# Optimization experiments

Measured on AMD Instinct MI355X. Metric: run time of the kernel, lower is better.

The kernel has to match this reference:

```python
import jax, jax.numpy as jnp
import numpy as np

N = 50000          # nodes
E = 800000         # edges
D_IN = 768         # LM embedding dim (hardcoded in SimpleHGN first conv)
H = 128            # hidden_dim
REL_DIM = 32       # hardcoded rel_dim
N_REL = 3          # n_relations
BETA = 0.05        # SimpleHGN_att_res
NEG_SLOPE = 0.2    # LeakyReLU in attention


def setup_inputs() -> dict:
    key = jax.random.key(0)
    ks = jax.random.split(key, 16)
    s = 0.05  # param init scale
    return {
        'x': jax.random.normal(ks[0], (N, D_IN), jnp.float32),
        'edge_index': jax.random.randint(ks[1], (2, E), 0, N, dtype=jnp.int64),
        'edge_type': jax.random.randint(ks[2], (E,), 0, N_REL, dtype=jnp.int64),
        'W0': jax.random.normal(ks[3], (D_IN, H), jnp.float32) * s,
        'Wr0': jax.random.normal(ks[4], (REL_DIM, H), jnp.float32) * s,
        'a0': jax.random.normal(ks[5], (3 * H, 1), jnp.float32) * s,
        'rel0': jax.random.normal(ks[6], (N_REL, REL_DIM), jnp.float32) * s,
        'W1': jax.random.normal(ks[7], (H, H), jnp.float32) * s,
        'Wr1': jax.random.normal(ks[8], (REL_DIM, H), jnp.float32) * s,
        'a1': jax.random.normal(ks[9], (3 * H, 1), jnp.float32) * s,
        'rel1': jax.random.normal(ks[10], (N_REL, REL_DIM), jnp.float32) * s,
        'pool_w': jax.random.normal(ks[11], (H, H), jnp.float32) * s,
        'pool_b': jnp.zeros((H,), jnp.float32),
        'out_w': jax.random.normal(ks[12], (H, 2), jnp.float32) * s,
        'out_b': jnp.zeros((2,), jnp.float32),
    }


def _hgn_conv(x, src, dst, et, W, Wr, a, rel, pre_alpha):
    """One SimpleHGNConv layer. Returns (ELU(aggregated), alpha detached)."""
    h = x @ W                                   # [N, H]
    r = rel[et] @ Wr                            # [E, H] edge-type embedding
    aw = a[:, 0]
    a_i, a_j, a_r = aw[:h.shape[1]], aw[h.shape[1]:2 * h.shape[1]], aw[2 * h.shape[1]:]
    # logits = leaky_relu(cat(h_i, h_j, r) @ a) computed without [E,3H] concat
    node_i = h @ a_i                            # [N]
    node_j = h @ a_j                            # [N]
    logit = jax.nn.leaky_relu(node_i[dst] + node_j[src] + r @ a_r, NEG_SLOPE)  # [E]
    # segment softmax over destination node neighborhoods (PyG softmax, +1e-16)
    m = jax.ops.segment_max(logit, dst, num_segments=N)
    e = jnp.exp(logit - m[dst])
    ssum = jax.ops.segment_sum(e, dst, num_segments=N)
    alpha = e / (ssum[dst] + 1e-16)             # [E]
    if pre_alpha is not None:
        alpha = alpha * (1.0 - BETA) + pre_alpha * BETA
    msg = h[src] * alpha[:, None]               # [E, H]
    out = jax.ops.segment_sum(msg, dst, num_segments=N)  # [N, H]
    return jax.nn.elu(out), jax.lax.stop_gradient(alpha)


def reference(x, edge_index, edge_type, W0, Wr0, a0, rel0, W1, Wr1, a1, rel1,
              pool_w, pool_b, out_w, out_b):
    src, dst = edge_index[0], edge_index[1]     # x_j = source, x_i = target
    h, alpha = _hgn_conv(x, src, dst, edge_type, W0, Wr0, a0, rel0, None)
    h, alpha = _hgn_conv(h, src, dst, edge_type, W1, Wr1, a1, rel1, alpha)
    # dropout is identity in eval; activation = relu per config
    h = jax.nn.relu(h @ pool_w + pool_b)
    return h @ out_w + out_b                    # [N, 2]
```

## Files before the change

kernel.cpp:

```cpp
#include <hip/hip_runtime.h>
#include <hip/hip_fp16.h>
#include <cstdint>
#include <cstddef>

#define N_NODES 50000
#define N_EDGES 800000
#define DIN_    768
#define H_DIM   128
#define N_REL   3
#define BETA_F  0.05f
#define SLOPE_F 0.2f

static inline int cdiv(int a, int b) { return (a + b - 1) / b; }

typedef __attribute__((ext_vector_type(8))) short bf16x8;
typedef __attribute__((ext_vector_type(8))) unsigned short u16x8;
typedef __attribute__((ext_vector_type(4))) float f32x4;

__device__ __forceinline__ unsigned short f2bf(float f) {
  unsigned u = __builtin_bit_cast(unsigned, f);
  unsigned r = (u + 0x7fffu + ((u >> 16) & 1u)) >> 16;
  return (unsigned short)r;
}
__device__ __forceinline__ float bf2f(unsigned short h) {
  unsigned u = ((unsigned)h) << 16;
  return __builtin_bit_cast(float, u);
}

#define GLOAD_LDS16(g, s) __builtin_amdgcn_global_load_lds( \
    (const __attribute__((address_space(1))) void*)(g),      \
    (__attribute__((address_space(3))) void*)(s), 16, 0, 0)

__global__ void k_count(const int* __restrict__ dst, int* __restrict__ deg, int E) {
  int e = blockIdx.x * blockDim.x + threadIdx.x;
  if (e < E) atomicAdd(&deg[dst[e]], 1);
}

__global__ __launch_bounds__(256) void k_scan1(const int* __restrict__ deg,
                                               int* __restrict__ part, int n) {
  __shared__ int wsum[4];
  int i = blockIdx.x * 256 + threadIdx.x;
  int lane = threadIdx.x & 63, w = threadIdx.x >> 6;
  int v = (i < n) ? deg[i] : 0;
  #pragma unroll
  for (int d = 32; d > 0; d >>= 1) v += __shfl_xor(v, d);
  if (lane == 0) wsum[w] = v;
  __syncthreads();
  if (threadIdx.x == 0) part[blockIdx.x] = wsum[0] + wsum[1] + wsum[2] + wsum[3];
}

__global__ __launch_bounds__(256) void k_scan2(int* __restrict__ part,
                                               int* __restrict__ off, int nb, int n) {
  __shared__ int sh[256];
  int t = threadIdx.x;
  int v = (t < nb) ? part[t] : 0;
  int incl = v;
  sh[t] = incl;
  __syncthreads();
  #pragma unroll
  for (int d = 1; d < 256; d <<= 1) {
    int u = (t >= d) ? sh[t - d] : 0;
    __syncthreads();
    sh[t] += u;
    __syncthreads();
  }
  incl = sh[t];
  if (t < nb) part[t] = incl - v;
  if (t == nb - 1) off[n] = incl;
}

__global__ __launch_bounds__(256) void k_scan3(const int* __restrict__ deg,
                                               const int* __restrict__ part,
                                               int* __restrict__ off,
                                               int* __restrict__ cur, int n) {
  __shared__ int wsum[4];
  int i = blockIdx.x * 256 + threadIdx.x;
  int lane = threadIdx.x & 63, w = threadIdx.x >> 6;
  int v = (i < n) ? deg[i] : 0;
  int incl = v;
  #pragma unroll
  for (int d = 1; d < 64; d <<= 1) {
    int u = __shfl_up(incl, d);
    if (lane >= d) incl += u;
  }
  if (lane == 63) wsum[w] = incl;
  __syncthreads();
  int woff = 0;
  #pragma unroll
  for (int k = 0; k < 4; ++k) woff += (k < w) ? wsum[k] : 0;
  int ex = incl - v + woff + part[blockIdx.x];
  if (i < n) { off[i] = ex; cur[i] = ex; }
}

__global__ void k_fill(const int* __restrict__ dst, int* __restrict__ cur,
                       int* __restrict__ csr, int E) {
  int e = blockIdx.x * blockDim.x + threadIdx.x;
  if (e < E) {
    int p = atomicAdd(&cur[dst[e]], 1);
    csr[p] = e;
  }
}

__global__ __launch_bounds__(128) void k_relscore(const float* __restrict__ rel,
                                                  const float* __restrict__ Wr,
                                                  const float* __restrict__ a,
                                                  float* __restrict__ rs) {
  __shared__ float red[128];
  int k = threadIdx.x;
  for (int t = 0; t < N_REL; ++t) {
    float p = 0.f;
    #pragma unroll
    for (int j = 0; j < 32; ++j) p += rel[t * 32 + j] * Wr[j * H_DIM + k];
    red[k] = p * a[2 * H_DIM + k];
    __syncthreads();
    for (int s = 64; s > 0; s >>= 1) {
      if (k < s) red[k] += red[k + s];
      __syncthreads();
    }
    if (k == 0) rs[t] = red[0];
    __syncthreads();
  }
}

__global__ void k_prep(const float* __restrict__ W, int K,
                       short* __restrict__ th, short* __restrict__ tl) {
  int id = blockIdx.x * 256 + threadIdx.x;
  if (id >= K * 128) return;
  int k = id >> 7, c = id & 127;
  float w = W[id];
  unsigned short h = f2bf(w);
  unsigned short l = f2bf(w - bf2f(h));
  int kt = k >> 5;
  int kk = k & 31;
  int g = kk >> 3, j = kk & 7;
  int p = g ^ (c & 3) ^ ((c >> 2) & 3);
  size_t pos = (size_t)kt * 4096 + c * 32 + p * 8 + j;
  th[pos] = (short)h;
  tl[pos] = (short)l;
}

template <bool BIASRELU, bool W16>
__global__ __launch_bounds__(256, 5) void k_gemm_mfma(const float* __restrict__ A,
                                                      const short* __restrict__ Bth,
                                                      const short* __restrict__ Btl,
                                                      const float* __restrict__ bias,
                                                      float* __restrict__ C,
                                                      __half* __restrict__ C16,
                                                      int n, int K) {
  __shared__ __align__(16) char sm[2][16384];
  int t = threadIdx.x;
  int l = t & 63, wid = t >> 6;
  int wr = wid >> 1, wc = wid & 1;
  int lr = l & 15, lk = l >> 4;
  int row0 = blockIdx.x * 64;

  f32x4 acc[2][4];
  #pragma unroll
  for (int m = 0; m < 2; ++m)
    #pragma unroll
    for (int nn = 0; nn < 4; ++nn) acc[m][nn] = (f32x4)(0.f);

  const int nt = K >> 5;

  const float* a_src0;
  const float* a_src1;
  {
    int s = wid;
    int r = s * 8 + (l >> 3);
    int gr = row0 + r; if (gr >= n) gr = n - 1;
    a_src0 = A + (size_t)gr * K + (((l & 7) ^ (r & 7)) << 2);
    s = 4 + wid;
    r = s * 8 + (l >> 3);
    gr = row0 + r; if (gr >= n) gr = n - 1;
    a_src1 = A + (size_t)gr * K + (((l & 7) ^ (r & 7)) << 2);
  }

  auto stage = [&](int it, char* buf) {
    int k0 = it << 5;
    const short* bh_t = Bth + (size_t)it * 4096;
    GLOAD_LDS16(a_src0 + k0,                    buf + wid * 1024);
    GLOAD_LDS16(a_src1 + k0,                    buf + (4 + wid) * 1024);
    GLOAD_LDS16(bh_t + wid * 512 + l * 8,       buf + 8192 + wid * 1024);
    GLOAD_LDS16(bh_t + (4 + wid) * 512 + l * 8, buf + 8192 + (4 + wid) * 1024);
  };

  auto compute = [&](int it, const char* buf) {
    const char* Ab = buf;
    const char* Bhb = buf + 8192;
    const short* bl_t = Btl + (size_t)it * 4096;
    bf16x8 ah[2], al[2], bh[4], bl[4];
    #pragma unroll
    for (int m = 0; m < 2; ++m) {
      int r = wr * 32 + m * 16 + lr;
      int g0 = (2 * lk) ^ (r & 7);
      int g1 = (2 * lk + 1) ^ (r & 7);
      float4 f0 = *(const float4*)(Ab + r * 128 + g0 * 16);
      float4 f1 = *(const float4*)(Ab + r * 128 + g1 * 16);
      float ff[8] = {f0.x, f0.y, f0.z, f0.w, f1.x, f1.y, f1.z, f1.w};
      u16x8 hv, lv;
      #pragma unroll
      for (int j = 0; j < 8; ++j) {
        unsigned u = __builtin_bit_cast(unsigned, ff[j]);
        unsigned short h = (unsigned short)(u >> 16);
        hv[j] = h;
        lv[j] = f2bf(ff[j] - bf2f(h));
      }
      ah[m] = __builtin_bit_cast(bf16x8, hv);
      al[m] = __builtin_bit_cast(bf16x8, lv);
    }
    #pragma unroll
    for (int nn = 0; nn < 4; ++nn) {
      int c = wc * 64 + nn * 16 + lr;
      int p = lk ^ (c & 3) ^ ((c >> 2) & 3);
      bh[nn] = *(const bf16x8*)(Bhb + c * 64 + p * 16);
      bl[nn] = *(const bf16x8*)(bl_t + c * 32 + p * 8);
    }
    #pragma unroll
    for (int m = 0; m < 2; ++m)
      #pragma unroll
      for (int nn = 0; nn < 4; ++nn) {
        acc[m][nn] = __builtin_amdgcn_mfma_f32_16x16x32_bf16(ah[m], bh[nn], acc[m][nn], 0, 0, 0);
        acc[m][nn] = __builtin_amdgcn_mfma_f32_16x16x32_bf16(ah[m], bl[nn], acc[m][nn], 0, 0, 0);
        acc[m][nn] = __builtin_amdgcn_mfma_f32_16x16x32_bf16(al[m], bh[nn], acc[m][nn], 0, 0, 0);
      }
  };

  stage(0, sm[0]);
  if (nt > 1) stage(1, sm[1]);

  for (int it = 0; it < nt; ++it) {
    if (it + 1 < nt) { asm volatile("s_waitcnt vmcnt(4)" ::: "memory"); }
    else             { asm volatile("s_waitcnt vmcnt(0)" ::: "memory"); }
    asm volatile("s_barrier" ::: "memory");
    compute(it, sm[it & 1]);
    asm volatile("s_barrier" ::: "memory");
    if (it + 2 < nt) stage(it + 2, sm[it & 1]);
  }

  #pragma unroll
  for (int m = 0; m < 2; ++m) {
    int rbase = row0 + wr * 32 + m * 16 + lk * 4;
    #pragma unroll
    for (int nn = 0; nn < 4; ++nn) {
      int c = wc * 64 + nn * 16 + lr;
      #pragma unroll
      for (int q = 0; q < 4; ++q) {
        int r = rbase + q;
        if (r < n) {
          float v = acc[m][nn][q];
          if (BIASRELU) {
            v += bias[c];
            v = v > 0.f ? v : 0.f;
          }
          C[(size_t)r * 128 + c] = v;
          if (W16) C16[(size_t)r * 128 + c] = __float2half(v);
        }
      }
    }
  }
}

__global__ __launch_bounds__(256) void k_scores(const float* __restrict__ h,
                                                const float* __restrict__ a,
                                                float* __restrict__ ni,
                                                float* __restrict__ nj, int n) {
  int lane = threadIdx.x & 63;
  int w = threadIdx.x >> 6;
  int row = blockIdx.x * 4 + w;
  if (row >= n) return;
  float2 v = ((const float2*)(h + (size_t)row * H_DIM))[lane];
  float2 ai = ((const float2*)a)[lane];
  float2 aj = ((const float2*)(a + H_DIM))[lane];
  float si = v.x * ai.x + v.y * ai.y;
  float sj = v.x * aj.x + v.y * aj.y;
  #pragma unroll
  for (int d = 32; d > 0; d >>= 1) {
    si += __shfl_xor(si, d);
    sj += __shfl_xor(sj, d);
  }
  if (lane == 0) { ni[row] = si; nj[row] = sj; }
}

__global__ void k_logit(const int* __restrict__ src, const int* __restrict__ dst,
                        const int* __restrict__ et,
                        const float* __restrict__ ni, const float* __restrict__ nj,
                        const float* __restrict__ rs,
                        float* __restrict__ logit, int E) {
  int e = blockIdx.x * blockDim.x + threadIdx.x;
  if (e >= E) return;
  float v = ni[dst[e]] + nj[src[e]] + rs[et[e]];
  logit[e] = v > 0.f ? v : SLOPE_F * v;
}

template <int LAYER>
__global__ __launch_bounds__(128) void k_aggregate(const int* __restrict__ off,
                                                   const int* __restrict__ csr,
                                                   const int* __restrict__ src,
                                                   const float* __restrict__ logit,
                                                   const __half* __restrict__ h16,
                                                   float* __restrict__ alpha_io,
                                                   float* __restrict__ hout, int n) {
  __shared__ float l_red[2];
  __shared__ float l_alpha[128];
  __shared__ int   l_src[128];
  int nid = blockIdx.x;
  int t = threadIdx.x;
  int lane = t & 63;
  int w = t >> 6;
  int start = off[nid];
  int deg = off[nid + 1] - start;
  float hv = 0.f;
  if (deg > 0) {
    float m = -INFINITY;
    for (int k = t; k < deg; k += 128) m = fmaxf(m, logit[csr[start + k]]);
    #pragma unroll
    for (int d = 32; d > 0; d >>= 1) m = fmaxf(m, __shfl_xor(m, d));
    if (lane == 0) l_red[w] = m;
    __syncthreads();
    m = fmaxf(l_red[0], l_red[1]);
    __syncthreads();
    float s = 0.f;
    for (int k = t; k < deg; k += 128) s += expf(logit[csr[start + k]] - m);
    #pragma unroll
    for (int d = 32; d > 0; d >>= 1) s += __shfl_xor(s, d);
    if (lane == 0) l_red[w] = s;
    __syncthreads();
    float denom = l_red[0] + l_red[1] + 1e-16f;
    for (int base = 0; base < deg; base += 128) {
      int kk = base + t;
      if (kk < deg) {
        int e = csr[start + kk];
        float al = expf(logit[e] - m) / denom;
        if (LAYER == 1) {
          al = al * (1.f - BETA_F) + BETA_F * alpha_io[e];
        } else {
          alpha_io[e] = al;
        }
        l_alpha[t] = al;
        l_src[t] = src[e];
      }
      __syncthreads();
      int cnt = deg - base; if (cnt > 128) cnt = 128;
      #pragma unroll 4
      for (int k = 0; k < cnt; ++k)
        hv += l_alpha[k] * __half2float(h16[(size_t)l_src[k] * H_DIM + t]);
      __syncthreads();
    }
  }
  hout[(size_t)nid * H_DIM + t] = hv > 0.f ? hv : expm1f(hv);
}

__global__ __launch_bounds__(256) void k_out(const float* __restrict__ P,
                                             const float* __restrict__ ow,
                                             const float* __restrict__ ob,
                                             float* __restrict__ out, int n) {
  int lane = threadIdx.x & 63;
  int w = threadIdx.x >> 6;
  int row = blockIdx.x * 4 + w;
  if (row >= n) return;
  float2 v  = ((const float2*)(P + (size_t)row * H_DIM))[lane];
  float2 w0 = ((const float2*)ow)[2 * lane];
  float2 w1 = ((const float2*)ow)[2 * lane + 1];
  float s0 = v.x * w0.x + v.y * w1.x;
  float s1 = v.x * w0.y + v.y * w1.y;
  #pragma unroll
  for (int d = 32; d > 0; d >>= 1) {
    s0 += __shfl_xor(s0, d);
    s1 += __shfl_xor(s1, d);
  }
  if (lane == 0) {
    out[row * 2]     = s0 + ob[0];
    out[row * 2 + 1] = s1 + ob[1];
  }
}

extern "C" void kernel_launch(void* const* d_in, const int* in_sizes, int n_in,
                              void* d_out, int out_size, void* d_ws, size_t ws_size,
                              hipStream_t stream) {
  const float* x      = (const float*)d_in[0];
  const int*   ei     = (const int*)d_in[1];
  const int*   et     = (const int*)d_in[2];
  const float* W0     = (const float*)d_in[3];
  const float* Wr0    = (const float*)d_in[4];
  const float* a0     = (const float*)d_in[5];
  const float* rel0   = (const float*)d_in[6];
  const float* W1     = (const float*)d_in[7];
  const float* Wr1    = (const float*)d_in[8];
  const float* a1     = (const float*)d_in[9];
  const float* rel1   = (const float*)d_in[10];
  const float* pool_w = (const float*)d_in[11];
  const float* pool_b = (const float*)d_in[12];
  const float* out_w  = (const float*)d_in[13];
  const float* out_b  = (const float*)d_in[14];

  const int* src = ei;
  const int* dst = ei + N_EDGES;

  char* p = (char*)d_ws;
  auto take = [&](size_t bytes) {
    char* r = p;
    p += (bytes + 511) & ~(size_t)511;
    return r;
  };
  int*   deg    = (int*)take((size_t)N_NODES * 4);
  int*   off    = (int*)take((size_t)(N_NODES + 1) * 4);
  int*   cur    = (int*)take((size_t)N_NODES * 4);
  int*   part   = (int*)take((size_t)256 * 4);
  int*   csr    = (int*)take((size_t)N_EDGES * 4);
  float* logit  = (float*)take((size_t)N_EDGES * 4);
  float* alpha0 = (float*)take((size_t)N_EDGES * 4);
  float* ni     = (float*)take((size_t)N_NODES * 4);
  float* nj     = (float*)take((size_t)N_NODES * 4);
  float* rs     = (float*)take(256);
  short* wt0h   = (short*)take((size_t)DIN_ * 128 * 2);
  short* wt0l   = (short*)take((size_t)DIN_ * 128 * 2);
  short* wt1h   = (short*)take((size_t)128 * 128 * 2);
  short* wt1l   = (short*)take((size_t)128 * 128 * 2);
  short* wph    = (short*)take((size_t)128 * 128 * 2);
  short* wpl    = (short*)take((size_t)128 * 128 * 2);
  float* big1   = (float*)take((size_t)N_NODES * H_DIM * 4);
  float* big2   = (float*)take((size_t)N_NODES * H_DIM * 4);
  __half* h16   = (__half*)take((size_t)N_NODES * H_DIM * 2);

  const int EB = cdiv(N_EDGES, 256);
  const int GB = cdiv(N_NODES, 64);
  const int SB = cdiv(N_NODES, 256);

  hipMemsetAsync(deg, 0, (size_t)N_NODES * 4, stream);
  k_count<<<EB, 256, 0, stream>>>(dst, deg, N_EDGES);
  k_scan1<<<SB, 256, 0, stream>>>(deg, part, N_NODES);
  k_scan2<<<1, 256, 0, stream>>>(part, off, SB, N_NODES);
  k_scan3<<<SB, 256, 0, stream>>>(deg, part, off, cur, N_NODES);
  k_fill<<<EB, 256, 0, stream>>>(dst, cur, csr, N_EDGES);

  k_prep<<<cdiv(DIN_ * 128, 256), 256, 0, stream>>>(W0, DIN_, wt0h, wt0l);
  k_prep<<<cdiv(128 * 128, 256), 256, 0, stream>>>(W1, 128, wt1h, wt1l);
  k_prep<<<cdiv(128 * 128, 256), 256, 0, stream>>>(pool_w, 128, wph, wpl);

  k_relscore<<<1, 128, 0, stream>>>(rel0, Wr0, a0, rs);
  k_gemm_mfma<false, true><<<GB, 256, 0, stream>>>(x, wt0h, wt0l, nullptr, big1, h16, N_NODES, DIN_);
  k_scores<<<cdiv(N_NODES, 4), 256, 0, stream>>>(big1, a0, ni, nj, N_NODES);
  k_logit<<<EB, 256, 0, stream>>>(src, dst, et, ni, nj, rs, logit, N_EDGES);
  k_aggregate<0><<<N_NODES, 128, 0, stream>>>(off, csr, src, logit, h16, alpha0, big2, N_NODES);

  k_relscore<<<1, 128, 0, stream>>>(rel1, Wr1, a1, rs);
  k_gemm_mfma<false, true><<<GB, 256, 0, stream>>>(big2, wt1h, wt1l, nullptr, big1, h16, N_NODES, 128);
  k_scores<<<cdiv(N_NODES, 4), 256, 0, stream>>>(big1, a1, ni, nj, N_NODES);
  k_logit<<<EB, 256, 0, stream>>>(src, dst, et, ni, nj, rs, logit, N_EDGES);
  k_aggregate<1><<<N_NODES, 128, 0, stream>>>(off, csr, src, logit, h16, alpha0, big2, N_NODES);

  k_gemm_mfma<true, false><<<GB, 256, 0, stream>>>(big2, wph, wpl, pool_b, big1, nullptr, N_NODES, 128);
  k_out<<<cdiv(N_NODES, 4), 256, 0, stream>>>(big1, out_w, out_b, (float*)d_out, N_NODES);
}
```

Before: 433.9 us.

## Store edge data in CSR order and stage low-part weights through LDS

k_fill now records each edge's CSR position and writes a CSR-sorted source array. k_logit scatters logits directly into CSR order, so k_aggregate reads logits, sources and alpha contiguously instead of through a csr indirection. Separately, the GEMM also stages the low bf16 weight tile into LDS, which enlarges shared memory and lowers launch bounds from 5 to 3 blocks per CU. This trades random gathers in the aggregation for a scattered write in k_logit and an extra position array. The GEMM change risks lower occupancy.

Result: faster. 381.6 us (-12.0%).

```diff
diff --git a/kernel.cpp b/kernel.cpp
--- a/kernel.cpp
+++ b/kernel.cpp
@@ -92,12 +92,14 @@
   if (i < n) { off[i] = ex; cur[i] = ex; }
 }
 
-__global__ void k_fill(const int* __restrict__ dst, int* __restrict__ cur,
-                       int* __restrict__ csr, int E) {
+__global__ void k_fill(const int* __restrict__ dst, const int* __restrict__ src,
+                       int* __restrict__ cur, int* __restrict__ pos,
+                       int* __restrict__ src_s, int E) {
   int e = blockIdx.x * blockDim.x + threadIdx.x;
   if (e < E) {
     int p = atomicAdd(&cur[dst[e]], 1);
-    csr[p] = e;
+    pos[e] = p;
+    src_s[p] = src[e];
   }
 }
 
@@ -140,14 +142,14 @@
 }
 
 template <bool BIASRELU, bool W16>
-__global__ __launch_bounds__(256, 5) void k_gemm_mfma(const float* __restrict__ A,
+__global__ __launch_bounds__(256, 3) void k_gemm_mfma(const float* __restrict__ A,
                                                       const short* __restrict__ Bth,
                                                       const short* __restrict__ Btl,
                                                       const float* __restrict__ bias,
                                                       float* __restrict__ C,
                                                       __half* __restrict__ C16,
                                                       int n, int K) {
-  __shared__ __align__(16) char sm[2][16384];
+  __shared__ __align__(16) char sm[2][24576];
   int t = threadIdx.x;
   int l = t & 63, wid = t >> 6;
   int wr = wid >> 1, wc = wid & 1;
@@ -178,16 +180,19 @@
   auto stage = [&](int it, char* buf) {
     int k0 = it << 5;
     const short* bh_t = Bth + (size_t)it * 4096;
+    const short* bl_t = Btl + (size_t)it * 4096;
     GLOAD_LDS16(a_src0 + k0,                    buf + wid * 1024);
     GLOAD_LDS16(a_src1 + k0,                    buf + (4 + wid) * 1024);
     GLOAD_LDS16(bh_t + wid * 512 + l * 8,       buf + 8192 + wid * 1024);
     GLOAD_LDS16(bh_t + (4 + wid) * 512 + l * 8, buf + 8192 + (4 + wid) * 1024);
+    GLOAD_LDS16(bl_t + wid * 512 + l * 8,       buf + 16384 + wid * 1024);
+    GLOAD_LDS16(bl_t + (4 + wid) * 512 + l * 8, buf + 16384 + (4 + wid) * 1024);
   };
 
-  auto compute = [&](int it, const char* buf) {
+  auto compute = [&](const char* buf) {
     const char* Ab = buf;
     const char* Bhb = buf + 8192;
-    const short* bl_t = Btl + (size_t)it * 4096;
+    const char* Blb = buf + 16384;
     bf16x8 ah[2], al[2], bh[4], bl[4];
     #pragma unroll
     for (int m = 0; m < 2; ++m) {
@@ -213,7 +218,7 @@
       int c = wc * 64 + nn * 16 + lr;
       int p = lk ^ (c & 3) ^ ((c >> 2) & 3);
       bh[nn] = *(const bf16x8*)(Bhb + c * 64 + p * 16);
-      bl[nn] = *(const bf16x8*)(bl_t + c * 32 + p * 8);
+      bl[nn] = *(const bf16x8*)(Blb + c * 64 + p * 16);
     }
     #pragma unroll
     for (int m = 0; m < 2; ++m)
@@ -229,10 +234,10 @@
   if (nt > 1) stage(1, sm[1]);
 
   for (int it = 0; it < nt; ++it) {
-    if (it + 1 < nt) { asm volatile("s_waitcnt vmcnt(4)" ::: "memory"); }
+    if (it + 1 < nt) { asm volatile("s_waitcnt vmcnt(6)" ::: "memory"); }
     else             { asm volatile("s_waitcnt vmcnt(0)" ::: "memory"); }
     asm volatile("s_barrier" ::: "memory");
-    compute(it, sm[it & 1]);
+    compute(sm[it & 1]);
     asm volatile("s_barrier" ::: "memory");
     if (it + 2 < nt) stage(it + 2, sm[it & 1]);
   }
@@ -284,21 +289,20 @@
 __global__ void k_logit(const int* __restrict__ src, const int* __restrict__ dst,
                         const int* __restrict__ et,
                         const float* __restrict__ ni, const float* __restrict__ nj,
-                        const float* __restrict__ rs,
-                        float* __restrict__ logit, int E) {
+                        const float* __restrict__ rs, const int* __restrict__ pos,
+                        float* __restrict__ logit_s, int E) {
   int e = blockIdx.x * blockDim.x + threadIdx.x;
   if (e >= E) return;
   float v = ni[dst[e]] + nj[src[e]] + rs[et[e]];
-  logit[e] = v > 0.f ? v : SLOPE_F * v;
+  logit_s[pos[e]] = v > 0.f ? v : SLOPE_F * v;
 }
 
 template <int LAYER>
 __global__ __launch_bounds__(128) void k_aggregate(const int* __restrict__ off,
-                                                   const int* __restrict__ csr,
-                                                   const int* __restrict__ src,
-                                                   const float* __restrict__ logit,
+                                                   const int* __restrict__ src_s,
+                                                   const float* __restrict__ logit_s,
                                                    const __half* __restrict__ h16,
-                                                   float* __restrict__ alpha_io,
+                                                   float* __restrict__ alpha_s,
                                                    float* __restrict__ hout, int n) {
   __shared__ float l_red[2];
   __shared__ float l_alpha[128];
@@ -312,7 +316,7 @@
   float hv = 0.f;
   if (deg > 0) {
     float m = -INFINITY;
-    for (int k = t; k < deg; k += 128) m = fmaxf(m, logit[csr[start + k]]);
+    for (int k = t; k < deg; k += 128) m = fmaxf(m, logit_s[start + k]);
     #pragma unroll
     for (int d = 32; d > 0; d >>= 1) m = fmaxf(m, __shfl_xor(m, d));
     if (lane == 0) l_red[w] = m;
@@ -320,7 +324,7 @@
     m = fmaxf(l_red[0], l_red[1]);
     __syncthreads();
     float s = 0.f;
-    for (int k = t; k < deg; k += 128) s += expf(logit[csr[start + k]] - m);
+    for (int k = t; k < deg; k += 128) s += expf(logit_s[start + k] - m);
     #pragma unroll
     for (int d = 32; d > 0; d >>= 1) s += __shfl_xor(s, d);
     if (lane == 0) l_red[w] = s;
@@ -329,15 +333,14 @@
     for (int base = 0; base < deg; base += 128) {
       int kk = base + t;
       if (kk < deg) {
-        int e = csr[start + kk];
-        float al = expf(logit[e] - m) / denom;
+        float al = expf(logit_s[start + kk] - m) / denom;
         if (LAYER == 1) {
-          al = al * (1.f - BETA_F) + BETA_F * alpha_io[e];
+          al = al * (1.f - BETA_F) + BETA_F * alpha_s[start + kk];
         } else {
-          alpha_io[e] = al;
+          alpha_s[start + kk] = al;
         }
         l_alpha[t] = al;
-        l_src[t] = src[e];
+        l_src[t] = src_s[start + kk];
       }
       __syncthreads();
       int cnt = deg - base; if (cnt > 128) cnt = 128;
@@ -402,25 +405,26 @@
     p += (bytes + 511) & ~(size_t)511;
     return r;
   };
-  int*   deg    = (int*)take((size_t)N_NODES * 4);
-  int*   off    = (int*)take((size_t)(N_NODES + 1) * 4);
-  int*   cur    = (int*)take((size_t)N_NODES * 4);
-  int*   part   = (int*)take((size_t)256 * 4);
-  int*   csr    = (int*)take((size_t)N_EDGES * 4);
-  float* logit  = (float*)take((size_t)N_EDGES * 4);
-  float* alpha0 = (float*)take((size_t)N_EDGES * 4);
-  float* ni     = (float*)take((size_t)N_NODES * 4);
-  float* nj     = (float*)take((size_t)N_NODES * 4);
-  float* rs     = (float*)take(256);
-  short* wt0h   = (short*)take((size_t)DIN_ * 128 * 2);
-  short* wt0l   = (short*)take((size_t)DIN_ * 128 * 2);
-  short* wt1h   = (short*)take((size_t)128 * 128 * 2);
-  short* wt1l   = (short*)take((size_t)128 * 128 * 2);
-  short* wph    = (short*)take((size_t)128 * 128 * 2);
-  short* wpl    = (short*)take((size_t)128 * 128 * 2);
-  float* big1   = (float*)take((size_t)N_NODES * H_DIM * 4);
-  float* big2   = (float*)take((size_t)N_NODES * H_DIM * 4);
-  __half* h16   = (__half*)take((size_t)N_NODES * H_DIM * 2);
+  int*   deg     = (int*)take((size_t)N_NODES * 4);
+  int*   off     = (int*)take((size_t)(N_NODES + 1) * 4);
+  int*   cur     = (int*)take((size_t)N_NODES * 4);
+  int*   part    = (int*)take((size_t)256 * 4);
+  int*   pos     = (int*)take((size_t)N_EDGES * 4);
+  int*   src_s   = (int*)take((size_t)N_EDGES * 4);
+  float* logit_s = (float*)take((size_t)N_EDGES * 4);
+  float* alpha_s = (float*)take((size_t)N_EDGES * 4);
+  float* ni      = (float*)take((size_t)N_NODES * 4);
+  float* nj      = (float*)take((size_t)N_NODES * 4);
+  float* rs      = (float*)take(256);
+  short* wt0h    = (short*)take((size_t)DIN_ * 128 * 2);
+  short* wt0l    = (short*)take((size_t)DIN_ * 128 * 2);
+  short* wt1h    = (short*)take((size_t)128 * 128 * 2);
+  short* wt1l    = (short*)take((size_t)128 * 128 * 2);
+  short* wph     = (short*)take((size_t)128 * 128 * 2);
+  short* wpl     = (short*)take((size_t)128 * 128 * 2);
+  float* big1    = (float*)take((size_t)N_NODES * H_DIM * 4);
+  float* big2    = (float*)take((size_t)N_NODES * H_DIM * 4);
+  __half* h16    = (__half*)take((size_t)N_NODES * H_DIM * 2);
 
   const int EB = cdiv(N_EDGES, 256);
   const int GB = cdiv(N_NODES, 64);
@@ -431,7 +435,7 @@
   k_scan1<<<SB, 256, 0, stream>>>(deg, part, N_NODES);
   k_scan2<<<1, 256, 0, stream>>>(part, off, SB, N_NODES);
   k_scan3<<<SB, 256, 0, stream>>>(deg, part, off, cur, N_NODES);
-  k_fill<<<EB, 256, 0, stream>>>(dst, cur, csr, N_EDGES);
+  k_fill<<<EB, 256, 0, stream>>>(dst, src, cur, pos, src_s, N_EDGES);
 
   k_prep<<<cdiv(DIN_ * 128, 256), 256, 0, stream>>>(W0, DIN_, wt0h, wt0l);
   k_prep<<<cdiv(128 * 128, 256), 256, 0, stream>>>(W1, 128, wt1h, wt1l);
@@ -440,14 +444,14 @@
   k_relscore<<<1, 128, 0, stream>>>(rel0, Wr0, a0, rs);
   k_gemm_mfma<false, true><<<GB, 256, 0, stream>>>(x, wt0h, wt0l, nullptr, big1, h16, N_NODES, DIN_);
   k_scores<<<cdiv(N_NODES, 4), 256, 0, stream>>>(big1, a0, ni, nj, N_NODES);
-  k_logit<<<EB, 256, 0, stream>>>(src, dst, et, ni, nj, rs, logit, N_EDGES);
-  k_aggregate<0><<<N_NODES, 128, 0, stream>>>(off, csr, src, logit, h16, alpha0, big2, N_NODES);
+  k_logit<<<EB, 256, 0, stream>>>(src, dst, et, ni, nj, rs, pos, logit_s, N_EDGES);
+  k_aggregate<0><<<N_NODES, 128, 0, stream>>>(off, src_s, logit_s, h16, alpha_s, big2, N_NODES);
 
   k_relscore<<<1, 128, 0, stream>>>(rel1, Wr1, a1, rs);
   k_gemm_mfma<false, true><<<GB, 256, 0, stream>>>(big2, wt1h, wt1l, nullptr, big1, h16, N_NODES, 128);
   k_scores<<<cdiv(N_NODES, 4), 256, 0, stream>>>(big1, a1, ni, nj, N_NODES);
-  k_logit<<<EB, 256, 0, stream>>>(src, dst, et, ni, nj, rs, logit, N_EDGES);
-  k_aggregate<1><<<N_NODES, 128, 0, stream>>>(off, csr, src, logit, h16, alpha0, big2, N_NODES);
+  k_logit<<<EB, 256, 0, stream>>>(src, dst, et, ni, nj, rs, pos, logit_s, N_EDGES);
+  k_aggregate<1><<<N_NODES, 128, 0, stream>>>(off, src_s, logit_s, h16, alpha_s, big2, N_NODES);
 
   k_gemm_mfma<true, false><<<GB, 256, 0, stream>>>(big2, wph, wpl, pool_b, big1, nullptr, N_NODES, 128);
   k_out<<<cdiv(N_NODES, 4), 256, 0, stream>>>(big1, out_w, out_b, (float*)d_out, N_NODES);
```
